# Optimization experiments

Hardware: AMD Instinct MI355X
Metric: run time of the kernel (lower is better)

The kernel has to match this reference:

```python
import jax, jax.numpy as jnp
import numpy as np
import math

N_VOX = 262144      # number of active voxels (input == output coords, stride=1)
C_IN = 64
C_OUT = 64
K_VOL = 27          # kernel_size**3
P_PER_OFF = 65536   # neighbor pairs per kernel offset (uniform nbsizes)


def setup_inputs() -> dict:
    key = jax.random.key(0)
    k1, k2, k3, k4 = jax.random.split(key, 4)
    feat = jax.random.normal(k1, (N_VOX, C_IN), dtype=jnp.float32)
    # reset_parameters: uniform(-std, std), std = 1/sqrt(in_channels * kernel_volume)
    std = 1.0 / math.sqrt(C_IN * K_VOL)
    kernel = jax.random.uniform(k2, (K_VOL, C_IN, C_OUT), dtype=jnp.float32,
                                minval=-std, maxval=std)
    src_ids = jax.random.randint(k3, (K_VOL, P_PER_OFF), 0, N_VOX, dtype=jnp.int32)
    tgt_ids = jax.random.randint(k4, (K_VOL, P_PER_OFF), 0, N_VOX, dtype=jnp.int32)
    return {"feat": feat, "kernel": kernel, "src_ids": src_ids, "tgt_ids": tgt_ids}


def reference(feat, kernel, src_ids, tgt_ids):
    # Sparse 3D conv (non-transposed): for each kernel offset k,
    #   out[tgt] += feat[src] @ kernel[k]
    # Gather per offset: [K, P, C_in]
    gathered = feat[src_ids]
    # Per-offset GEMM: [K, P, C_out]
    prod = jnp.einsum('kpi,kio->kpo', gathered, kernel)
    # Scatter-add into output voxels: [N_out, C_out]
    out = jax.ops.segment_sum(prod.reshape(-1, C_OUT), tgt_ids.reshape(-1),
                              num_segments=N_VOX)
    return out
```

## Files before the change

kernel.cpp:

```cpp
#include <hip/hip_runtime.h>

#define N_VOX 262144
#define C 64
#define K_VOL 27
#define P_PER_OFF 65536

#define WAVES_PER_BLOCK 4
#define BLOCK (WAVES_PER_BLOCK * 64)
#define PAIRS_PER_WAVE 256
#define BLOCKS_PER_K (P_PER_OFF / (PAIRS_PER_WAVE * WAVES_PER_BLOCK))

typedef __attribute__((ext_vector_type(16))) float f32x16;

__global__ __launch_bounds__(BLOCK) void conv_scatter(
    const float* __restrict__ feat,
    const float* __restrict__ kern,
    const int* __restrict__ src_ids,
    const int* __restrict__ tgt_ids,
    float* __restrict__ out)
{
    const int k    = blockIdx.y;
    const int wave = threadIdx.x >> 6;
    const int lane = threadIdx.x & 63;
    const int pbase = (blockIdx.x * WAVES_PER_BLOCK + wave) * PAIRS_PER_WAVE;

    float w[C];
    #pragma unroll
    for (int i = 0; i < C; ++i)
        w[i] = kern[(size_t)k * C * C + (size_t)i * C + lane];

    const int* sp = src_ids + (size_t)k * P_PER_OFF + pbase;
    const int* tp = tgt_ids + (size_t)k * P_PER_OFF + pbase;

    for (int j0 = 0; j0 < PAIRS_PER_WAVE; j0 += 64) {
        int sv = sp[j0 + lane];
        int tv = tp[j0 + lane];

        #pragma unroll 2
        for (int j = 0; j < 64; ++j) {
            int usrc = __builtin_amdgcn_readlane(sv, j);
            int utgt = __builtin_amdgcn_readlane(tv, j);

            const float* frow = feat + (size_t)usrc * C;

            f32x16 fa, fb, fc, fd;
            asm volatile(
                "s_load_dwordx16 %0, %4, 0x0\n\t"
                "s_load_dwordx16 %1, %4, 0x40\n\t"
                "s_load_dwordx16 %2, %4, 0x80\n\t"
                "s_load_dwordx16 %3, %4, 0xc0\n\t"
                "s_waitcnt lgkmcnt(0)"
                : "=&s"(fa), "=&s"(fb), "=&s"(fc), "=&s"(fd)
                : "s"(frow));

            float a0 = 0.f, a1 = 0.f, a2 = 0.f, a3 = 0.f;
            #pragma unroll
            for (int i = 0; i < 16; ++i) {
                a0 = fmaf(fa[i], w[i],      a0);
                a1 = fmaf(fb[i], w[16 + i], a1);
                a2 = fmaf(fc[i], w[32 + i], a2);
                a3 = fmaf(fd[i], w[48 + i], a3);
            }
            float r = (a0 + a1) + (a2 + a3);

            unsafeAtomicAdd(out + (size_t)utgt * C + lane, r);
        }
    }
}

extern "C" void kernel_launch(void* const* d_in, const int* in_sizes, int n_in,
                              void* d_out, int out_size, void* d_ws, size_t ws_size,
                              hipStream_t stream)
{
    const float* feat = (const float*)d_in[0];
    const float* kern = (const float*)d_in[1];
    const int*   src  = (const int*)d_in[2];
    const int*   tgt  = (const int*)d_in[3];
    float* out = (float*)d_out;

    hipMemsetAsync(out, 0, (size_t)N_VOX * C * sizeof(float), stream);

    dim3 grid(BLOCKS_PER_K, K_VOL);
    conv_scatter<<<grid, BLOCK, 0, stream>>>(feat, kern, src, tgt, out);
}
```

Before: 576.5 us.

## Use bf16x3 split MFMA for per-offset GEMM with prefetched gathers

Replaces the per-pair scalar-load FMA dot products with 16x16x32 bf16 MFMA tiles. Features and weights are split into hi/lo bf16 parts and combined with three MFMAs to keep near-fp32 accuracy. Each wave handles 16 pairs per batch with vector gathers and prefetches the next batch's source rows and target ids. This trades extra conversion work and 3x MFMA count for much less scalar ALU work. The atomic scatter traffic stays the same.

After: 470.7 us. -18.4%, faster.

```diff
diff --git a/kernel.cpp b/kernel.cpp
--- a/kernel.cpp
+++ b/kernel.cpp
@@ -3,16 +3,28 @@
 #define N_VOX 262144
 #define C 64
 #define K_VOL 27
-#define P_PER_OFF 65536
+#define P 65536
 
-#define WAVES_PER_BLOCK 4
-#define BLOCK (WAVES_PER_BLOCK * 64)
+#define BLOCK 256
+#define WAVES 4
 #define PAIRS_PER_WAVE 256
-#define BLOCKS_PER_K (P_PER_OFF / (PAIRS_PER_WAVE * WAVES_PER_BLOCK))
+#define NBATCH 16
+#define BLOCKS_PER_K (P / (PAIRS_PER_WAVE * WAVES))
 
-typedef __attribute__((ext_vector_type(16))) float f32x16;
+typedef __attribute__((ext_vector_type(8))) short bf16x8;
+typedef __attribute__((ext_vector_type(4))) float f32x4;
 
-__global__ __launch_bounds__(BLOCK) void conv_scatter(
+__device__ inline unsigned short cvt_bf16_rne(float x) {
+    unsigned u = __builtin_bit_cast(unsigned, x);
+    u += 0x7fff + ((u >> 16) & 1);
+    return (unsigned short)(u >> 16);
+}
+__device__ inline float bf16f(unsigned short h) {
+    unsigned u = (unsigned)h << 16;
+    return __builtin_bit_cast(float, u);
+}
+
+__global__ __launch_bounds__(BLOCK) void conv_mfma(
     const float* __restrict__ feat,
     const float* __restrict__ kern,
     const int* __restrict__ src_ids,
@@ -22,48 +34,98 @@
     const int k    = blockIdx.y;
     const int wave = threadIdx.x >> 6;
     const int lane = threadIdx.x & 63;
-    const int pbase = (blockIdx.x * WAVES_PER_BLOCK + wave) * PAIRS_PER_WAVE;
+    const int g    = lane >> 4;
+    const int col  = lane & 15;
 
-    float w[C];
-    #pragma unroll
-    for (int i = 0; i < C; ++i)
-        w[i] = kern[(size_t)k * C * C + (size_t)i * C + lane];
+    bf16x8 Bhi[2][4], Blo[2][4];
+    {
+        const float* Wk = kern + (size_t)k * C * C;
+        #pragma unroll
+        for (int kt = 0; kt < 2; ++kt)
+            #pragma unroll
+            for (int nt = 0; nt < 4; ++nt)
+                #pragma unroll
+                for (int i = 0; i < 8; ++i) {
+                    float w = Wk[(size_t)(kt * 32 + g * 8 + i) * C + nt * 16 + col];
+                    unsigned short h = cvt_bf16_rne(w);
+                    Bhi[kt][nt][i] = (short)h;
+                    Blo[kt][nt][i] = (short)cvt_bf16_rne(w - bf16f(h));
+                }
+    }
 
-    const int* sp = src_ids + (size_t)k * P_PER_OFF + pbase;
-    const int* tp = tgt_ids + (size_t)k * P_PER_OFF + pbase;
+    const int pb0 = (blockIdx.x * WAVES + wave) * PAIRS_PER_WAVE;
+    const int* srcp = src_ids + (size_t)k * P + pb0;
+    const int* tgtp = tgt_ids + (size_t)k * P + pb0;
 
-    for (int j0 = 0; j0 < PAIRS_PER_WAVE; j0 += 64) {
-        int sv = sp[j0 + lane];
-        int tv = tp[j0 + lane];
+    f32x4 ra0, ra1, ra2, ra3;
+    int tg0, tg1, tg2, tg3;
 
-        #pragma unroll 2
-        for (int j = 0; j < 64; ++j) {
-            int usrc = __builtin_amdgcn_readlane(sv, j);
-            int utgt = __builtin_amdgcn_readlane(tv, j);
+    int sv = srcp[col];
+    {
+        const float* fr = feat + (size_t)sv * C + g * 8;
+        ra0 = *(const f32x4*)(fr);
+        ra1 = *(const f32x4*)(fr + 4);
+        ra2 = *(const f32x4*)(fr + 32);
+        ra3 = *(const f32x4*)(fr + 36);
+    }
+    int sv_n = srcp[16 + col];
+    tg0 = tgtp[g * 4 + 0];
+    tg1 = tgtp[g * 4 + 1];
+    tg2 = tgtp[g * 4 + 2];
+    tg3 = tgtp[g * 4 + 3];
 
-            const float* frow = feat + (size_t)usrc * C;
+    for (int b = 0; b < NBATCH; ++b) {
+        bf16x8 Ahi[2], Alo[2];
+        #pragma unroll
+        for (int i = 0; i < 4; ++i) {
+            float x0 = ra0[i], x1 = ra1[i], x2 = ra2[i], x3 = ra3[i];
+            unsigned short h;
+            h = cvt_bf16_rne(x0); Ahi[0][i]     = (short)h; Alo[0][i]     = (short)cvt_bf16_rne(x0 - bf16f(h));
+            h = cvt_bf16_rne(x1); Ahi[0][4 + i] = (short)h; Alo[0][4 + i] = (short)cvt_bf16_rne(x1 - bf16f(h));
+            h = cvt_bf16_rne(x2); Ahi[1][i]     = (short)h; Alo[1][i]     = (short)cvt_bf16_rne(x2 - bf16f(h));
+            h = cvt_bf16_rne(x3); Ahi[1][4 + i] = (short)h; Alo[1][4 + i] = (short)cvt_bf16_rne(x3 - bf16f(h));
+        }
 
-            f32x16 fa, fb, fc, fd;
-            asm volatile(
-                "s_load_dwordx16 %0, %4, 0x0\n\t"
-                "s_load_dwordx16 %1, %4, 0x40\n\t"
-                "s_load_dwordx16 %2, %4, 0x80\n\t"
-                "s_load_dwordx16 %3, %4, 0xc0\n\t"
-                "s_waitcnt lgkmcnt(0)"
-                : "=&s"(fa), "=&s"(fb), "=&s"(fc), "=&s"(fd)
-                : "s"(frow));
+        const int ctg0 = tg0, ctg1 = tg1, ctg2 = tg2, ctg3 = tg3;
+        if (b + 1 < NBATCH) {
+            const int* tp = tgtp + (b + 1) * 16 + g * 4;
+            tg0 = tp[0]; tg1 = tp[1]; tg2 = tp[2]; tg3 = tp[3];
+        }
 
-            float a0 = 0.f, a1 = 0.f, a2 = 0.f, a3 = 0.f;
+        if (b + 1 < NBATCH) {
+            const float* fr = feat + (size_t)sv_n * C + g * 8;
+            ra0 = *(const f32x4*)(fr);
+            ra1 = *(const f32x4*)(fr + 4);
+            ra2 = *(const f32x4*)(fr + 32);
+            ra3 = *(const f32x4*)(fr + 36);
+            if (b + 2 < NBATCH) sv_n = srcp[(b + 2) * 16 + col];
+        }
+
+        f32x4 acc[4] = {f32x4{0.f,0.f,0.f,0.f}, f32x4{0.f,0.f,0.f,0.f},
+                        f32x4{0.f,0.f,0.f,0.f}, f32x4{0.f,0.f,0.f,0.f}};
+        #pragma unroll
+        for (int kt = 0; kt < 2; ++kt) {
             #pragma unroll
-            for (int i = 0; i < 16; ++i) {
-                a0 = fmaf(fa[i], w[i],      a0);
-                a1 = fmaf(fb[i], w[16 + i], a1);
-                a2 = fmaf(fc[i], w[32 + i], a2);
-                a3 = fmaf(fd[i], w[48 + i], a3);
-            }
-            float r = (a0 + a1) + (a2 + a3);
+            for (int nt = 0; nt < 4; ++nt)
+                acc[nt] = __builtin_amdgcn_mfma_f32_16x16x32_bf16(Ahi[kt], Bhi[kt][nt], acc[nt], 0, 0, 0);
+            #pragma unroll
+            for (int nt = 0; nt < 4; ++nt)
+                acc[nt] = __builtin_amdgcn_mfma_f32_16x16x32_bf16(Alo[kt], Bhi[kt][nt], acc[nt], 0, 0, 0);
+            #pragma unroll
+            for (int nt = 0; nt < 4; ++nt)
+                acc[nt] = __builtin_amdgcn_mfma_f32_16x16x32_bf16(Ahi[kt], Blo[kt][nt], acc[nt], 0, 0, 0);
+        }
 
-            unsafeAtomicAdd(out + (size_t)utgt * C + lane, r);
+        float* o0 = out + (size_t)ctg0 * C + col;
+        float* o1 = out + (size_t)ctg1 * C + col;
+        float* o2 = out + (size_t)ctg2 * C + col;
+        float* o3 = out + (size_t)ctg3 * C + col;
+        #pragma unroll
+        for (int nt = 0; nt < 4; ++nt) {
+            unsafeAtomicAdd(o0 + nt * 16, acc[nt][0]);
+            unsafeAtomicAdd(o1 + nt * 16, acc[nt][1]);
+            unsafeAtomicAdd(o2 + nt * 16, acc[nt][2]);
+            unsafeAtomicAdd(o3 + nt * 16, acc[nt][3]);
         }
     }
 }
@@ -81,5 +143,5 @@
     hipMemsetAsync(out, 0, (size_t)N_VOX * C * sizeof(float), stream);
 
     dim3 grid(BLOCKS_PER_K, K_VOL);
-    conv_scatter<<<grid, BLOCK, 0, stream>>>(feat, kern, src, tgt, out);
+    conv_mfma<<<grid, BLOCK, 0, stream>>>(feat, kern, src, tgt, out);
 }
```
